# Kernel tuning notes

Measured on AMD Instinct MI355X. Metric: run time of the kernel, lower is better.

The kernel has to match this reference:

```python
import jax, jax.numpy as jnp
import numpy as np

PAD, UNK, START, END = 0, 1, 2, 3


def _lstm_scan(x_tbd, Wih, Whh, b, reverse=False):
    # x_tbd: [T,B,Din]; returns all hidden states [T,B,H] and final hidden [B,H]
    B = x_tbd.shape[1]
    Hh = Whh.shape[1]
    def step(carry, xt):
        h, c = carry
        g = xt @ Wih.T + h @ Whh.T + b  # torch gate order i,f,g,o
        i, f, gg, o = jnp.split(g, 4, axis=-1)
        c = jax.nn.sigmoid(f) * c + jax.nn.sigmoid(i) * jnp.tanh(gg)
        h = jax.nn.sigmoid(o) * jnp.tanh(c)
        return (h, c), h
    z = jnp.zeros((B, Hh), x_tbd.dtype)
    (hT, _), hs = jax.lax.scan(step, (z, z), x_tbd, reverse=reverse)
    return hs, hT


def _forward(fl, input_ids, target_ids, target_lengths):
    (emb,
     eWih0f, eWhh0f, eb0f, eWih0b, eWhh0b, eb0b,
     eWih1f, eWhh1f, eb1f, eWih1b, eWhh1b, eb1b,
     dWih0, dWhh0, db0, dWih1, dWhh1, db1,
     Wenc, Wdec, Wvoc, sW, sb, ob) = fl
    V = emb.shape[0]
    B, S = input_ids.shape
    T = target_ids.shape[1]
    D = 2 * eWhh0f.shape[1]  # decoder hidden = 2*hidden_dim
    safe = lambda ids: jnp.where(ids >= V, UNK, ids)

    # ---- bidirectional 2-layer encoder ----
    x = emb[safe(input_ids)].transpose(1, 0, 2)  # [S,B,E]
    h0f, hf0T = _lstm_scan(x, eWih0f, eWhh0f, eb0f)
    h0b, hb0T = _lstm_scan(x, eWih0b, eWhh0b, eb0b, reverse=True)
    x1 = jnp.concatenate([h0f, h0b], -1)
    h1f, hf1T = _lstm_scan(x1, eWih1f, eWhh1f, eb1f)
    h1b, hb1T = _lstm_scan(x1, eWih1b, eWhh1b, eb1b, reverse=True)
    enc_hs = jnp.concatenate([h1f, h1b], -1).transpose(1, 0, 2)  # [B,S,D]
    # decoder init hidden: concat fwd/bwd final hidden per layer -> [2,B,D]
    dec_h0 = jnp.stack([jnp.concatenate([hf0T, hb0T], -1),
                        jnp.concatenate([hf1T, hb1T], -1)])

    out_proj = jnp.tanh(emb[END:] @ Wvoc)  # [V-3, 3D]
    pad_mask = input_ids == PAD
    t_range = jnp.arange(T)

    def cell(xx, h, c, Wih, Whh, b):
        g = xx @ Wih.T + h @ Whh.T + b
        i, f, gg, o = jnp.split(g, 4, -1)
        c = jax.nn.sigmoid(f) * c + jax.nn.sigmoid(i) * jnp.tanh(gg)
        return jax.nn.sigmoid(o) * jnp.tanh(c), c

    def step(carry, xs):
        h, c, cum, hist, cur, nll = carry
        t, nt = xs  # t scalar step index, nt [B] teacher tokens
        xx = emb[cur]
        h0, c0 = cell(xx, h[0], c[0], dWih0, dWhh0, db0)
        h1, c1 = cell(h0, h[1], c[1], dWih1, dWhh1, db1)
        # intra-temporal encoder attention
        s = jnp.minimum(jnp.einsum('bd,bsd->bs', h1 @ Wenc, enc_hs), 30.0)
        e = jnp.exp(s)
        temporal = e / jnp.where(t == 0, 1.0, cum + 1e-8)
        attn = jax.nn.softmax(jnp.where(pad_mask, -jnp.inf, temporal), axis=1)
        enc_ctx = jnp.einsum('bs,bsd->bd', attn, enc_hs)
        # intra-decoder attention over previous decoder hidden states
        ds = jnp.where(t_range[None, :] < t,
                       jnp.einsum('bd,ubd->bu', h1 @ Wdec, hist), -1e9)
        dec_ctx = jnp.where(t > 0,
                            jnp.einsum('bu,ubd->bd', jax.nn.softmax(ds, axis=1), hist),
                            0.0)
        concat = jnp.concatenate([h1, enc_ctx, dec_ctx], -1)  # [B,3D]
        vocab_dist = jax.nn.softmax(concat @ out_proj.T + ob, axis=1)  # [B,V-3]
        p_gen = jax.nn.sigmoid(concat @ sW.T + sb)[:, 0]
        # generation prob of teacher token (F.pad left by END zeros)
        idx = jnp.clip(nt - END, 0, V - END - 1)
        gen_p = jnp.where((nt >= END) & (nt < V),
                          jnp.take_along_axis(vocab_dist, idx[:, None], 1)[:, 0], 0.0)
        copy_p = jnp.sum(attn * (input_ids == nt[:, None]), axis=1)
        p = p_gen * gen_p + (1.0 - p_gen) * copy_p
        nll = nll - jnp.where(t < target_lengths, jnp.log(p + 1e-9), 0.0)
        return (jnp.stack([h0, h1]), jnp.stack([c0, c1]), cum + e,
                hist.at[t].set(h1), safe(nt), nll), None

    init = (dec_h0, jnp.zeros_like(dec_h0), jnp.zeros((B, S), emb.dtype),
            jnp.zeros((T, B, D), emb.dtype),
            jnp.full((B,), START), jnp.zeros((B,), emb.dtype))
    (_, _, _, _, _, nll), _ = jax.lax.scan(step, init, (t_range, target_ids.T))
    return nll  # per-example teacher-forcing NLL, shape [B]


def setup_inputs():
    key = jax.random.key(0)
    ks = jax.random.split(key, 40)
    B, S, T = 16, 512, 128
    V, E, H = 32000, 128, 256
    D = 2 * H
    inp = {}
    inp['input_ids'] = jax.random.randint(ks[0], (B, S), 4, V)      # no pad/special ids
    inp['target_ids'] = jax.random.randint(ks[1], (B, T), 4, V)
    inp['input_lengths'] = jnp.full((B,), S, dtype=jnp.int32)       # full-length (packing is identity)
    inp['target_lengths'] = jax.random.randint(ks[2], (B,), T // 2, T + 1)
    inp['max_num_oovs'] = 0
    def xav(k, shape):
        fan = shape[0] + shape[-1]
        return jax.random.normal(k, shape, jnp.float32) * np.sqrt(2.0 / fan)
    def lstm_b(n4):
        b = np.zeros(n4, np.float32)
        b[n4 // 4:n4 // 2] = 1.0  # forget-gate bias init
        return jnp.asarray(b)
    i = 3
    inp['emb'] = jax.random.uniform(ks[i], (V, E), jnp.float32, -0.1, 0.1); i += 1
    for l, din in [(0, E), (1, D)]:
        for d in 'fb':
            inp[f'enc_Wih_l{l}{d}'] = xav(ks[i], (4 * H, din)); i += 1
            inp[f'enc_Whh_l{l}{d}'] = xav(ks[i], (4 * H, H)); i += 1
            inp[f'enc_b_l{l}{d}'] = lstm_b(4 * H)
    for l, din in [(0, E), (1, D)]:
        inp[f'dec_Wih_l{l}'] = xav(ks[i], (4 * D, din)); i += 1
        inp[f'dec_Whh_l{l}'] = xav(ks[i], (4 * D, D)); i += 1
        inp[f'dec_b_l{l}'] = lstm_b(4 * D)
    inp['Wenc_attn'] = xav(ks[i], (D, D)); i += 1
    inp['Wdec_attn'] = xav(ks[i], (D, D)); i += 1
    inp['vocab_proj'] = xav(ks[i], (E, 6 * H)); i += 1
    inp['switch_W'] = xav(ks[i], (1, 6 * H)); i += 1
    inp['switch_b'] = jnp.zeros((1,), jnp.float32)
    inp['out_bias'] = jnp.zeros((V - 3,), jnp.float32)
    return inp


def reference(input_ids, target_ids, input_lengths, target_lengths, max_num_oovs,
              emb,
              enc_Wih_l0f, enc_Whh_l0f, enc_b_l0f, enc_Wih_l0b, enc_Whh_l0b, enc_b_l0b,
              enc_Wih_l1f, enc_Whh_l1f, enc_b_l1f, enc_Wih_l1b, enc_Whh_l1b, enc_b_l1b,
              dec_Wih_l0, dec_Whh_l0, dec_b_l0, dec_Wih_l1, dec_Whh_l1, dec_b_l1,
              Wenc_attn, Wdec_attn, vocab_proj, switch_W, switch_b, out_bias):
    # input_lengths unused (all full length -> pack/pad identity); max_num_oovs only
    # widens the zero-padded tail of the generator distribution (gathered probs unchanged).
    fl = (emb,
          enc_Wih_l0f, enc_Whh_l0f, enc_b_l0f, enc_Wih_l0b, enc_Whh_l0b, enc_b_l0b,
          enc_Wih_l1f, enc_Whh_l1f, enc_b_l1f, enc_Wih_l1b, enc_Whh_l1b, enc_b_l1b,
          dec_Wih_l0, dec_Whh_l0, dec_b_l0, dec_Wih_l1, dec_Whh_l1, dec_b_l1,
          Wenc_attn, Wdec_attn, vocab_proj, switch_W, switch_b, out_bias)
    return _forward(fl, input_ids, target_ids, target_lengths)
```

## Files before the change

### kernel.cpp

```cpp
#include <hip/hip_runtime.h>
#include <hip/hip_bf16.h>
#include <math.h>

#define PAD_ID 0
#define UNK_ID 1
#define START_ID 2
#define END_ID 3

constexpr int B = 16, S = 512, T = 128, V = 32000, E = 128, H = 256, D = 512;
constexpr int C3 = 1536;
constexpr int VO = 31997;
constexpr int JS = 32000;

typedef short short8 __attribute__((ext_vector_type(8)));
typedef float f32x4 __attribute__((ext_vector_type(4)));

__device__ __forceinline__ float sigm(float x) { return 1.0f / (1.0f + __expf(-x)); }
__device__ __forceinline__ short bf16s(float x) {
    __hip_bfloat16 h = __float2bfloat16(x);
    return *reinterpret_cast<short*>(&h);
}

__device__ __forceinline__ uint4 cloadu4(const uint* p) {
    uint4 v;
    asm volatile("global_load_dwordx4 %0, %1, off sc0 sc1" : "=v"(v) : "v"(p));
    return v;
}
__device__ __forceinline__ void pstore(uint* p, uint v) {
    __hip_atomic_store(p, v, __ATOMIC_RELAXED, __HIP_MEMORY_SCOPE_AGENT);
}

__device__ __forceinline__ void gload_lds16(const void* g, void* l) {
    __builtin_amdgcn_global_load_lds(
        (const __attribute__((address_space(1))) void*)(g),
        (__attribute__((address_space(3))) void*)(l), 16, 0, 0);
}

__device__ __forceinline__ void st_bf8(ushort* dst, float4 a, float4 b) {
    short8 o;
    o[0] = bf16s(a.x); o[1] = bf16s(a.y); o[2] = bf16s(a.z); o[3] = bf16s(a.w);
    o[4] = bf16s(b.x); o[5] = bf16s(b.y); o[6] = bf16s(b.z); o[7] = bf16s(b.w);
    *(short8*)dst = o;
}

__device__ __forceinline__ void poll_stage16(const uint* src, uint e, ushort* dst) {
    uint4 a0, a1, a2, a3;
    for (;;) {
        a0 = cloadu4(src); a1 = cloadu4(src + 4); a2 = cloadu4(src + 8); a3 = cloadu4(src + 12);
        asm volatile("s_waitcnt vmcnt(0)" ::: "memory");
        __builtin_amdgcn_sched_barrier(0);
        uint d = (a0.x ^ e) | (a0.y ^ e) | (a0.z ^ e) | (a0.w ^ e)
               | (a1.x ^ e) | (a1.y ^ e) | (a1.z ^ e) | (a1.w ^ e)
               | (a2.x ^ e) | (a2.y ^ e) | (a2.z ^ e) | (a2.w ^ e)
               | (a3.x ^ e) | (a3.y ^ e) | (a3.z ^ e) | (a3.w ^ e);
        if ((d & 0xffffu) == 0) break;
        __builtin_amdgcn_s_sleep(1);
    }
    short8 o0, o1;
    o0[0] = (short)(a0.x >> 16); o0[1] = (short)(a0.y >> 16); o0[2] = (short)(a0.z >> 16); o0[3] = (short)(a0.w >> 16);
    o0[4] = (short)(a1.x >> 16); o0[5] = (short)(a1.y >> 16); o0[6] = (short)(a1.z >> 16); o0[7] = (short)(a1.w >> 16);
    o1[0] = (short)(a2.x >> 16); o1[1] = (short)(a2.y >> 16); o1[2] = (short)(a2.z >> 16); o1[3] = (short)(a2.w >> 16);
    o1[4] = (short)(a3.x >> 16); o1[5] = (short)(a3.y >> 16); o1[6] = (short)(a3.z >> 16); o1[7] = (short)(a3.w >> 16);
    *(short8*)dst = o0;
    *(short8*)(dst + 8) = o1;
}

__device__ __forceinline__ void poll_stage32(const uint* src, uint e, ushort* dst) {
    uint4 a[8];
    for (;;) {
#pragma unroll
        for (int i = 0; i < 8; i++) a[i] = cloadu4(src + i * 4);
        asm volatile("s_waitcnt vmcnt(0)" ::: "memory");
        __builtin_amdgcn_sched_barrier(0);
        uint d = 0;
#pragma unroll
        for (int i = 0; i < 8; i++)
            d |= (a[i].x ^ e) | (a[i].y ^ e) | (a[i].z ^ e) | (a[i].w ^ e);
        if ((d & 0xffffu) == 0) break;
        __builtin_amdgcn_s_sleep(1);
    }
#pragma unroll
    for (int i = 0; i < 8; i += 2) {
        short8 o;
        o[0] = (short)(a[i].x >> 16);     o[1] = (short)(a[i].y >> 16);
        o[2] = (short)(a[i].z >> 16);     o[3] = (short)(a[i].w >> 16);
        o[4] = (short)(a[i + 1].x >> 16); o[5] = (short)(a[i + 1].y >> 16);
        o[6] = (short)(a[i + 1].z >> 16); o[7] = (short)(a[i + 1].w >> 16);
        *(short8*)(dst + i * 4) = o;
    }
}

__global__ void pack4_kernel(const float* __restrict__ W, float4* __restrict__ P, int Hn, int K) {
    int i = blockIdx.x * blockDim.x + threadIdx.x;
    if (i >= K * Hn) return;
    int k = i / Hn, u = i - k * Hn;
    float4 v;
    v.x = W[(size_t)(0 * Hn + u) * K + k];
    v.y = W[(size_t)(1 * Hn + u) * K + k];
    v.z = W[(size_t)(2 * Hn + u) * K + k];
    v.w = W[(size_t)(3 * Hn + u) * K + k];
    P[(size_t)k * Hn + u] = v;
}

__global__ void packencMK_k(const float* __restrict__ W, ushort* __restrict__ P, int K) {
    int i = blockIdx.x * blockDim.x + threadIdx.x;
    if (i >= 4 * H * K) return;
    int k = i % K, row = i / K;
    int g = (row >> 3) & 3, ul = row & 7, uh = row >> 5;
    int u = uh * 8 + ul;
    P[i] = (ushort)bf16s(W[(size_t)(g * H + u) * K + k]);
}

__global__ void packdecM_k(const float* __restrict__ W, ushort* __restrict__ P) {
    int i = blockIdx.x * blockDim.x + threadIdx.x;
    if (i >= 4 * D * D) return;
    int k = i & 511, row = i >> 9;
    int g = (row >> 4) & 3, u = (row >> 6) * 16 + (row & 15);
    P[i] = (ushort)bf16s(W[(size_t)(g * D + u) * D + k]);
}

__global__ void packdecM2_k(const float* __restrict__ Wi, const float* __restrict__ Wh,
                            ushort* __restrict__ P) {
    int i = blockIdx.x * blockDim.x + threadIdx.x;
    if (i >= 4 * D * D * 2) return;
    int k = i & 1023, row = i >> 10;
    int g = (row >> 4) & 3, u = (row >> 6) * 16 + (row & 15);
    float v = (k < 512) ? Wi[(size_t)(g * D + u) * D + k]
                        : Wh[(size_t)(g * D + u) * D + (k - 512)];
    P[i] = (ushort)bf16s(v);
}

__global__ void enc0_gates2(const int* __restrict__ ids, const float* __restrict__ emb,
                            const float4* __restrict__ Pf, const float* __restrict__ bf_,
                            const float4* __restrict__ Pb, const float* __restrict__ bb_,
                            float* __restrict__ Gf, float* __restrict__ Gb) {
    int n0 = blockIdx.x * 8;
    int u = threadIdx.x;
    __shared__ float xr[8][E];
    for (int i = u; i < 8 * E; i += 256) {
        int r = i >> 7, e = i & 127;
        int n = n0 + r, s = n / B, b = n - s * B;
        int tok = ids[b * S + s];
        if (tok >= V) tok = UNK_ID;
        xr[r][e] = emb[(size_t)tok * E + e];
    }
    __syncthreads();
#pragma unroll
    for (int dir = 0; dir < 2; dir++) {
        const float4* P = dir ? Pb : Pf;
        const float* bs = dir ? bb_ : bf_;
        float* G = dir ? Gb : Gf;
        float acc[8][4];
#pragma unroll
        for (int r = 0; r < 8; r++)
#pragma unroll
            for (int g = 0; g < 4; g++) acc[r][g] = 0.f;
#pragma unroll 4
        for (int k = 0; k < E; k++) {
            float4 w = P[k * H + u];
#pragma unroll
            for (int r = 0; r < 8; r++) {
                float x = xr[r][k];
                acc[r][0] += x * w.x; acc[r][1] += x * w.y;
                acc[r][2] += x * w.z; acc[r][3] += x * w.w;
            }
        }
        float b0 = bs[u], b1 = bs[H + u], b2 = bs[2 * H + u], b3 = bs[3 * H + u];
#pragma unroll
        for (int r = 0; r < 8; r++) {
            float* g = G + (size_t)(n0 + r) * (4 * H);
            g[u] = acc[r][0] + b0; g[H + u] = acc[r][1] + b1;
// ... 136 lines not shown
                acc0 = __builtin_amdgcn_mfma_f32_16x16x32_bf16(afr[0][kt], bfr, acc0, 0, 0, 0);
                acc1 = __builtin_amdgcn_mfma_f32_16x16x32_bf16(afr[1][kt], bfr, acc1, 0, 0, 0);
            }
#pragma unroll
            for (int i = 0; i < 4; i++) {
                gs[w][hi * 4 + i][cl] = acc0[i];
                gs[w][16 + hi * 4 + i][cl] = acc1[i];
            }
        }
        __syncthreads();
        {
            float q0 = gs[gsw][0 + ul][bb];
            float q1 = gs[gsw][8 + ul][bb];
            float q2 = gs[gsw][16 + ul][bb];
            float q3 = gs[gsw][24 + ul][bb];
            float ig = sigm(pa0 + q0), fg = sigm(pa1 + q1), gt = tanhf(pa2 + q2), og = sigm(pa3 + q3);
            c_a = fg * c_a + ig * gt;
            float hA = og * tanhf(c_a);
            q0 = gs[gsw][0 + ul][bb + 8];
            q1 = gs[gsw][8 + ul][bb + 8];
            q2 = gs[gsw][16 + ul][bb + 8];
            q3 = gs[gsw][24 + ul][bb + 8];
            ig = sigm(pb0 + q0); fg = sigm(pb1 + q1); gt = tanhf(pb2 + q2); og = sigm(pb3 + q3);
            c_b = fg * c_b + ig * gt;
            float hB = og * tanhf(c_b);
            uint tg = (uint)(step + 1) & 0xffffu;
            uint* dstp = pk + (cur ^ 1) * 8192 + dirb * 4096;
            pstore(&dstp[bb * 256 + u_glob], ((uint)(ushort)bf16s(hA) << 16) | tg);
            pstore(&dstp[(bb + 8) * 256 + u_glob], ((uint)(ushort)bf16s(hB) << 16) | tg);
            ho[((size_t)(s * B + bb)) * H + u_glob] = hA;
            ho[((size_t)(s * B + bb + 8)) * H + u_glob] = hB;
            if (step == S - 1) {
                hfin[bb * (2 * H) + dirb * H + u_glob] = hA;
                hfin[(bb + 8) * (2 * H) + dirb * H + u_glob] = hB;
            }
        }
    }
}

__device__ __forceinline__ void dec0_body(int bid, char* smem,
        const int* __restrict__ tgt, const float* __restrict__ emb,
        const float4* __restrict__ P, const float* __restrict__ bias,
        float* __restrict__ G) {
    float (*xr)[E] = (float(*)[E])smem;
    int n0 = bid * 8;
    int tid = threadIdx.x;
    for (int i = tid; i < 8 * E; i += 256) {
        int r = i >> 7, e = i & 127;
        int n = n0 + r, t = n / B, b = n - t * B;
        int tok;
        if (t == 0) tok = START_ID;
        else { tok = tgt[b * T + (t - 1)]; if (tok >= V) tok = UNK_ID; }
        xr[r][e] = emb[(size_t)tok * E + e];
    }
    __syncthreads();
#pragma unroll
    for (int half = 0; half < 2; half++) {
        int u = tid + half * 256;
        float acc[8][4];
#pragma unroll
        for (int r = 0; r < 8; r++)
#pragma unroll
            for (int g = 0; g < 4; g++) acc[r][g] = 0.f;
#pragma unroll 4
        for (int k = 0; k < E; k++) {
            float4 w = P[k * D + u];
#pragma unroll
            for (int r = 0; r < 8; r++) {
                float x = xr[r][k];
                acc[r][0] += x * w.x; acc[r][1] += x * w.y;
                acc[r][2] += x * w.z; acc[r][3] += x * w.w;
            }
        }
        float b0 = bias[u], b1 = bias[D + u], b2 = bias[2 * D + u], b3 = bias[3 * D + u];
#pragma unroll
        for (int r = 0; r < 8; r++) {
            float* g = G + (size_t)(n0 + r) * (4 * D);
            g[u] = acc[r][0] + b0; g[D + u] = acc[r][1] + b1;
            g[2 * D + u] = acc[r][2] + b2; g[3 * D + u] = acc[r][3] + b3;
        }
    }
}

__device__ __forceinline__ void dec_body(int bk, char* smem,
        const float* __restrict__ G0, const ushort* __restrict__ PM0,
        const ushort* __restrict__ PM1, const float* __restrict__ b1,
        uint* __restrict__ h0pk, uint* __restrict__ h1pk,
        float* __restrict__ h1out) {
    ushort* hb = (ushort*)smem;
    float (*gs)[16][17] = (float(*)[16][17])(smem + 33024);
    int tid = threadIdx.x;
    int lane = tid & 63, w = tid >> 6;
    int cl = lane & 15, hi = lane >> 4;

    short8 a0[16], a1[32];
    {
        const ushort* base0 = PM0 + (size_t)(bk * 64 + w * 16 + cl) * 512 + hi * 8;
#pragma unroll
        for (int kt = 0; kt < 16; kt++) a0[kt] = *(const short8*)(base0 + kt * 32);
        const ushort* base1 = PM1 + (size_t)(bk * 64 + w * 16 + cl) * 1024 + hi * 8;
#pragma unroll
        for (int kt = 0; kt < 32; kt++) a1[kt] = *(const short8*)(base1 + kt * 32);
    }
    int u_loc = tid & 15, b = tid >> 4;
    int u = bk * 16 + u_loc;
    float bi0 = b1[u], bi1 = b1[512 + u], bi2 = b1[1024 + u], bi3 = b1[1536 + u];
    float c0v = 0.f, c1v = 0.f;
    int sb = tid >> 4, kseg = tid & 15;
    int sflat = sb * 512 + kseg * 32;

    for (int t = 0; t < T; t++) {
        int cur = t & 1;
        poll_stage32(h0pk + ((t + 1) & 1) * 8192 + sflat, (uint)(t + 1) & 0xffffu,
                     hb + sb * 1032 + kseg * 32);
        __syncthreads();
        {
            f32x4 acc = {0.f, 0.f, 0.f, 0.f};
            const ushort* hp = hb + cl * 1032 + hi * 8;
#pragma unroll
            for (int kt = 0; kt < 16; kt++) {
                short8 bfr = *(const short8*)(hp + kt * 32);
                acc = __builtin_amdgcn_mfma_f32_16x16x32_bf16(a0[kt], bfr, acc, 0, 0, 0);
            }
#pragma unroll
            for (int i = 0; i < 4; i++) gs[w][hi * 4 + i][cl] = acc[i];
        }
        __syncthreads();
        {
            const float* gg = G0 + ((size_t)(t * B + b)) * 2048 + u;
            float g0 = gg[0]    + gs[0][u_loc][b];
            float g1 = gg[512]  + gs[1][u_loc][b];
            float g2 = gg[1024] + gs[2][u_loc][b];
            float g3 = gg[1536] + gs[3][u_loc][b];
            float ig = sigm(g0), fg = sigm(g1), gt = tanhf(g2), og = sigm(g3);
            c0v = fg * c0v + ig * gt;
            float h0n = og * tanhf(c0v);
            pstore(&h0pk[cur * 8192 + b * 512 + u],
                   ((uint)(ushort)bf16s(h0n) << 16) | ((uint)(t + 2) & 0xffffu));
        }
        poll_stage32(h0pk + cur * 8192 + sflat, (uint)(t + 2) & 0xffffu,
                     hb + sb * 1032 + kseg * 32);
        poll_stage32(h1pk + ((t + 1) & 1) * 8192 + sflat, (uint)(t + 1) & 0xffffu,
                     hb + sb * 1032 + 512 + kseg * 32);
        __syncthreads();
        {
            f32x4 acc = {0.f, 0.f, 0.f, 0.f};
            const ushort* hp = hb + cl * 1032 + hi * 8;
#pragma unroll
            for (int kt = 0; kt < 32; kt++) {
                short8 bfr = *(const short8*)(hp + kt * 32);
                acc = __builtin_amdgcn_mfma_f32_16x16x32_bf16(a1[kt], bfr, acc, 0, 0, 0);
            }
#pragma unroll
            for (int i = 0; i < 4; i++) gs[w][hi * 4 + i][cl] = acc[i];
        }
        __syncthreads();
        {
            float g0 = bi0 + gs[0][u_loc][b];
            float g1 = bi1 + gs[1][u_loc][b];
            float g2 = bi2 + gs[2][u_loc][b];
            float g3 = bi3 + gs[3][u_loc][b];
            float ig = sigm(g0), fg = sigm(g1), gt = tanhf(g2), og = sigm(g3);
            c1v = fg * c1v + ig * gt;
            float h1n = og * tanhf(c1v);
            pstore(&h1pk[cur * 8192 + b * 512 + u],
                   ((uint)(ushort)bf16s(h1n) << 16) | ((uint)(t + 2) & 0xffffu));
            h1out[((size_t)(t * B + b)) * 512 + u] = h1n;
        }
        __syncthreads();
    }
}

__device__ __forceinline__ void encht2_body(int bid,
        const float* __restrict__ h1f, const float* __restrict__ h1b,
        ushort* __restrict__ enchB) {
    int idx = bid * 256 + threadIdx.x;
    int b = idx >> 15;
    int r = idx & 32767;
    int o = r >> 9, s = r & 511;
    const float* src = (o < 32) ? (h1f + ((size_t)(s * B + b)) * H + o * 8)
                                : (h1b + ((size_t)(s * B + b)) * H + (o - 32) * 8);
    float4 v0 = *(const float4*)src, v1 = *(const float4*)(src + 4);
    st_bf8(enchB + ((size_t)b << 18) + o * 4096 + s * 8, v0, v1);
}

__device__ __forceinline__ void encht2T_body(int bid,
        const float* __restrict__ h1f, const float* __restrict__ h1b,
        ushort* __restrict__ enchT) {
    int idx = bid * 256 + threadIdx.x;
    int b = idx >> 15;
    int r = idx & 32767;
    int o = r >> 9, d = r & 511;
    float f[8];
#pragma unroll
    for (int j = 0; j < 8; j++) {
        int s = o * 8 + j;
        f[j] = (d < H) ? h1f[((size_t)(s * B + b)) * H + d]
                       : h1b[((size_t)(s * B + b)) * H + (d - H)];
    }
    float4 v0 = {f[0], f[1], f[2], f[3]}, v1 = {f[4], f[5], f[6], f[7]};
    st_bf8(enchT + ((size_t)b << 18) + o * 4096 + d * 8, v0, v1);
}

__device__ __forceinline__ void outproj_body(int bid, char* smem,
        const float* __restrict__ emb, const float* __restrict__ Wvoc,
        __hip_bfloat16* __restrict__ outT2) {
    float (*er)[E + 1] = (float(*)[E + 1])smem;
    int j0 = bid * 32;
    int jl = threadIdx.x & 31, oq = threadIdx.x >> 5;
    for (int i = threadIdx.x; i < 32 * E; i += 256) {
        int jj = i >> 7, e = i & 127;
        int j = j0 + jj;
        er[jj][e] = (j < VO) ? emb[(size_t)(3 + j) * E + e] : 0.f;
    }
    __syncthreads();
    int j = j0 + jl;
#pragma unroll 1
    for (int i = 0; i < 24; i++) {
        int o = oq * 24 + i;
        int k0 = o * 8;
        float acc[8];
#pragma unroll
        for (int kk = 0; kk < 8; kk++) acc[kk] = 0.f;
#pragma unroll 4
        for (int e = 0; e < E; e++) {
            float x = er[jl][e];
            float4 w0 = *(const float4*)(Wvoc + (size_t)e * C3 + k0);
            float4 w1 = *(const float4*)(Wvoc + (size_t)e * C3 + k0 + 4);
            acc[0] += x * w0.x; acc[1] += x * w0.y; acc[2] += x * w0.z; acc[3] += x * w0.w;
            acc[4] += x * w1.x; acc[5] += x * w1.y; acc[6] += x * w1.z; acc[7] += x * w1.w;
        }
        short8 v;
#pragma unroll
        for (int kk = 0; kk < 8; kk++) v[kk] = bf16s(tanhf(acc[kk]));
        *reinterpret_cast<short8*>((char*)outT2 + ((size_t)o * JS + j) * 16) = v;
    }
}

template<int NF, int TILES, int OSTR, bool DOEXP>
__device__ __forceinline__ void gemm16_body(char* smem,
        const ushort* __restrict__ Abase, int arow_stride,
        const ushort* __restrict__ Bsrc, float* __restrict__ outbase,
        int out_stride) {
    ushort* Bs = (ushort*)smem;
    const int CH = NF * 64;
    const int NG = CH / 64;
    int tid = threadIdx.x;
    int lane = tid & 63, w = tid >> 6;
    int cl = lane & 15, hi = lane >> 4;
    short8 a[NF];
    {
        const ushort* asrc = Abase + (size_t)(w * 16 + cl) * arow_stride + hi * 8;
#pragma unroll
        for (int kt = 0; kt < NF; kt++) a[kt] = *(const short8*)(asrc + kt * 32);
    }
    for (int g = w; g < NG; g += 8) {
        int c = g * 64 + lane;
        int o = c >> 4, jl = c & 15;
        gload_lds16(Bsrc + ((size_t)o * OSTR + jl) * 8,
                    (char*)Bs + (size_t)(g * 64) * 16);
    }
    asm volatile("s_waitcnt vmcnt(0)" ::: "memory");
    __syncthreads();
    int buf = 0;
    for (int t = 0; t < TILES; t++) {
        if (t + 1 < TILES) {
            for (int g = w; g < NG; g += 8) {
                int c = g * 64 + lane;
                int o = c >> 4, jl = c & 15;
                gload_lds16(Bsrc + ((size_t)o * OSTR + (t + 1) * 16 + jl) * 8,
                            (char*)Bs + (size_t)((buf ^ 1) * CH + g * 64) * 16);
            }
        }
        f32x4 acc = {0.f, 0.f, 0.f, 0.f};
        const ushort* bp = Bs + (size_t)buf * CH * 8 + (size_t)(hi * 16 + cl) * 8;
#pragma unroll
        for (int kt = 0; kt < NF; kt++) {
            short8 b = *(const short8*)(bp + (size_t)kt * 512);
            acc = __builtin_amdgcn_mfma_f32_16x16x32_bf16(a[kt], b, acc, 0, 0, 0);
        }
#pragma unroll
        for (int i = 0; i < 4; i++) {
            int row = w * 16 + hi * 4 + i;
            float v = acc[i];
            if (DOEXP) v = __expf(fminf(v, 30.0f));
            outbase[(size_t)row * out_stride + t * 16 + cl] = v;
        }
        asm volatile("s_waitcnt vmcnt(0)" ::: "memory");
        __syncthreads();
        buf ^= 1;
    }
}


__global__ void __launch_bounds__(256) megaA(
        const float* Gf, const float* Gb, const ushort* PMf, const ushort* PMb,
        float* hof, float* hob, float* hfin, uint* pk,
        const int* tgt, const float* emb, const float4* PdW, const float* dbias,
        float* Gd0) {
    __shared__ __align__(16) char smem[17152];
    int blk = blockIdx.x;
    if (blk < 16) enc_scan_body(blk, smem, Gf, Gb, PMf, PMb, hof, hob, hfin, pk);
    else dec0_body(blk - 16, smem, tgt, emb, PdW, dbias, Gd0);
}

__global__ void __launch_bounds__(256) enc_pscan3(
        const float* Gf, const float* Gb, const ushort* PMf, const ushort* PMb,
        float* hof, float* hob, float* hfin, uint* pk) {
    __shared__ __align__(16) char smem[17152];
    enc_scan_body(blockIdx.x, smem, Gf, Gb, PMf, PMb, hof, hob, hfin, pk);
}

__global__ void __launch_bounds__(256) megaC(
        const float* G0, const ushort* PM0, const ushort* PM1, const float* b1,
        uint* h0pk, uint* h1pk, float* h1out,
        const float* h1f, const float* h1b, ushort* enchB, ushort* enchT,
        const float* emb, const float* Wvoc, __hip_bfloat16* outT2) {
    __shared__ __align__(16) char smem[37376];
    int blk = blockIdx.x;
    if (blk < 32) dec_body(blk, smem, G0, PM0, PM1, b1, h0pk, h1pk, h1out);
    else if (blk < 2080) encht2_body(blk - 32, h1f, h1b, enchB);
    else if (blk < 4128) encht2T_body(blk - 2080, h1f, h1b, enchT);
    else outproj_body(blk - 4128, smem, emb, Wvoc, outT2);
}

__global__ void dec_initpk(const float* __restrict__ hinit,
                           uint* __restrict__ h0pk, uint* __restrict__ h1pk) {
    int i = blockIdx.x * blockDim.x + threadIdx.x;
    if (i >= B * D) return;
    pstore(&h0pk[8192 + i], ((uint)(ushort)bf16s(hinit[i]) << 16) | 1u);
    pstore(&h1pk[8192 + i], ((uint)(ushort)bf16s(hinit[B * D + i]) << 16) | 1u);
}

__global__ void qproj(const float* __restrict__ h1d, const float* __restrict__ Wenc,
                      const float* __restrict__ Wdec, ushort* __restrict__ qeb16,
                      ushort* __restrict__ qdb16, ushort* __restrict__ h1dB1) {
    int n = blockIdx.x;
    int o = threadIdx.x;
    __shared__ float hr[D];
    hr[o] = h1d[(size_t)n * D + o];
    __syncthreads();
    float ae = 0.f, ad = 0.f;
#pragma unroll 4
    for (int k = 0; k < D; k++) {
        float hk = hr[k];
        ae += hk * Wenc[k * D + o];
        ad += hk * Wdec[k * D + o];
    }
    int b = n & 15, t = n >> 4;
    size_t rowb = (size_t)(b * 128 + t) << 9;
    qeb16[rowb + o] = (ushort)bf16s(ae);
    qdb16[rowb + o] = (ushort)bf16s(ad);
    if (o < 64) {
        float4 v0 = *(const float4*)(hr + o * 8);
        float4 v1 = *(const float4*)(hr + o * 8 + 4);
        st_bf8(h1dB1 + ((size_t)b << 16) + o * 1024 + t * 8, v0, v1);
    }
}

__global__ void pack_h1dB2(const float* __restrict__ h1d, ushort* __restrict__ h1dB2) {
    int idx = blockIdx.x * 256 + threadIdx.x;
    int b = idx >> 13;
    int r = idx & 8191;
    int o = r >> 9, d = r & 511;
    float f[8];
#pragma unroll
    for (int j = 0; j < 8; j++)
        f[j] = h1d[((size_t)((o * 8 + j) * B + b)) * D + d];
    float4 v0 = {f[0], f[1], f[2], f[3]}, v1 = {f[4], f[5], f[6], f[7]};
    st_bf8(h1dB2 + ((size_t)b << 16) + o * 4096 + d * 8, v0, v1);
}

__global__ void __launch_bounds__(512) scoreAB(
        const ushort* __restrict__ qeb16, const ushort* __restrict__ enchB,
        float* __restrict__ ew,
        const ushort* __restrict__ qdb16, const ushort* __restrict__ h1dB1,
        float* __restrict__ dsout) {
    __shared__ __align__(16) char smem[32768];
    int blk = blockIdx.x;
    if (blk < 16) {
        int b = blk;
        gemm16_body<16, 32, 512, true>(smem,
            qeb16 + ((size_t)(b * 128) << 9), 512,
            enchB + ((size_t)b << 18),
            ew + (size_t)b * T * S, S);
    } else {
        int b = blk - 16;
        gemm16_body<16, 8, 128, false>(smem,
            qdb16 + ((size_t)(b * 128) << 9), 512,
            h1dB1 + ((size_t)b << 16),
            dsout + ((size_t)(b * 128)) * 128, 128);
    }
}

__global__ void temporal_k(float* __restrict__ ew) {
    int i = blockIdx.x * blockDim.x + threadIdx.x;
    if (i >= B * S) return;
    int b = i / S, sx = i - b * S;
    float cum = 0.f;
    for (int t = 0; t < T; t++) {
        size_t idx = ((size_t)(b * T + t)) * S + sx;
        float v = ew[idx];
        ew[idx] = v / (t == 0 ? 1.0f : (cum + 1e-8f));
        cum += v;
    }
}

__global__ void __launch_bounds__(512) smAB(
        const float* __restrict__ ew, const int* __restrict__ ids,
        const int* __restrict__ tgt, ushort* __restrict__ awb16,
        float* __restrict__ copyp,
        const float* __restrict__ dsout, ushort* __restrict__ pdb16) {
    __shared__ float red[512];
    int blk = blockIdx.x;
// ... 192 lines not shown
        float mn = fmaxf(M, mq);
        SS = SS * __expf(M - mn) + sq * __expf(mq - mn);
        M = mn;
        GL = fmaxf(GL, gq);
    }
    int nt = tgt[row];
    float genp = (nt >= 3 && nt < V) ? __expf(GL - M) / SS : 0.f;
    float pg = pgen[row];
    float p = pg * genp + (1.f - pg) * copyp[row];
    __shared__ float red[128];
    red[t] = (t < tlen[b]) ? -logf(p + 1e-9f) : 0.f;
    __syncthreads();
    for (int w = 64; w > 0; w >>= 1) { if (t < w) red[t] += red[t + w]; __syncthreads(); }
    if (t == 0) out[b] = red[0];
}

extern "C" void kernel_launch(void* const* d_in, const int* in_sizes, int n_in,
                              void* d_out, int out_size, void* d_ws, size_t ws_size,
                              hipStream_t stream) {
    const int* input_ids = (const int*)d_in[0];
    const int* target_ids = (const int*)d_in[1];
    const int* tlen = (const int*)d_in[3];
    const float* emb = (const float*)d_in[5];
    const float* eWih0f = (const float*)d_in[6],  *eWhh0f = (const float*)d_in[7],  *eb0f = (const float*)d_in[8];
    const float* eWih0b = (const float*)d_in[9],  *eWhh0b = (const float*)d_in[10], *eb0b = (const float*)d_in[11];
    const float* eWih1f = (const float*)d_in[12], *eWhh1f = (const float*)d_in[13], *eb1f = (const float*)d_in[14];
    const float* eWih1b = (const float*)d_in[15], *eWhh1b = (const float*)d_in[16], *eb1b = (const float*)d_in[17];
    const float* dWih0 = (const float*)d_in[18], *dWhh0 = (const float*)d_in[19], *db0 = (const float*)d_in[20];
    const float* dWih1 = (const float*)d_in[21], *dWhh1 = (const float*)d_in[22], *db1 = (const float*)d_in[23];
    const float* Wenc = (const float*)d_in[24], *Wdec = (const float*)d_in[25];
    const float* Wvoc = (const float*)d_in[26], *sW = (const float*)d_in[27], *sb = (const float*)d_in[28];
    const float* ob = (const float*)d_in[29];
    float* out = (float*)d_out;
    (void)ws_size; (void)n_in; (void)in_sizes; (void)out_size;

    char* A = (char*)d_ws;
    float4* pWih0f = (float4*)(A + 0);
    float4* pWih0b = (float4*)(A + 524288);
    ushort* PMW1f  = (ushort*)(A + 1048576);
    ushort* PMW1b  = (ushort*)(A + 2097152);
    float4* pdWih0 = (float4*)(A + 5242880);
    ushort* PMf0  = (ushort*)(A + 6291456);
    ushort* PMb0  = (ushort*)(A + 6815744);
    ushort* PMf1  = (ushort*)(A + 7340032);
    ushort* PMb1  = (ushort*)(A + 7864320);
    float* G0f = (float*)(A + 23068672);
    float* G0b = (float*)(A + 56623104);
    __hip_bfloat16* outT2 = (__hip_bfloat16*)A;

    char* Bh = A + 98304000;
    float* h0f = (float*)(Bh + 0);
    float* h0b = (float*)(Bh + 8388608);
    float* h1d = (float*)(Bh + 0);
    ushort* qeb16 = (ushort*)(Bh + 4194304);
    ushort* awb16 = (ushort*)(Bh + 6291456);
    ushort* qdb16 = (ushort*)(Bh + 8388608);
    ushort* h1dB1 = (ushort*)(Bh + 10485760);
    float* ew  = (float*)(Bh + 12582912);
    float* pbuf = (float*)(Bh + 12582912);

    char* Cr = Bh + 16777216;
    float* h1f = (float*)(Cr + 0);
    float* h1b = (float*)(Cr + 8388608);
    ushort* ccb16 = (ushort*)(Cr + 16777216);
    float*  dsout = (float*)(Cr + 23068672);
    ushort* pdb16 = (ushort*)(Cr + 24117248);
    ushort* h1dB2 = (ushort*)(Cr + 24641536);
    float* dec_init = (float*)(Cr + 29360128);
    float* pgen  = (float*)(Cr + 29425664);
    float* copyp = (float*)(Cr + 29433856);
    uint* hpkE0  = (uint*)(Cr + 29769728);
    uint* hpkE1  = (uint*)(Cr + 29835264);
    uint* h0pkD  = (uint*)(Cr + 29900800);
    uint* h1pkD  = (uint*)(Cr + 29966336);

    char* X = Cr + 30031872;
    float*  Gd0x  = (float*)(X + 0);
    ushort* PM0x  = (ushort*)(X + 16777216);
    ushort* PM1x  = (ushort*)(X + 18874368);
    ushort* enchB = (ushort*)(X + 23068672);
    float*  ectx  = (float*)(X + 31457280);
    float*  dctx  = (float*)(X + 35651584);
    ushort* enchT = (ushort*)(X + 39845888);

    hipMemsetAsync(hpkE0, 0, 262144, stream);

    auto pack = [&](const float* W, float4* P, int Hn, int K) {
        int total = Hn * K;
        hipLaunchKernelGGL(pack4_kernel, dim3((total + 255) / 256), dim3(256), 0, stream, W, P, Hn, K);
    };
    pack(eWih0f, pWih0f, H, E);
    pack(eWih0b, pWih0b, H, E);
    pack(dWih0, pdWih0, D, E);
    hipLaunchKernelGGL(packencMK_k, dim3(4 * H * 256 / 256), dim3(256), 0, stream, eWhh0f, PMf0, 256);
    hipLaunchKernelGGL(packencMK_k, dim3(4 * H * 256 / 256), dim3(256), 0, stream, eWhh0b, PMb0, 256);
    hipLaunchKernelGGL(packencMK_k, dim3(4 * H * 256 / 256), dim3(256), 0, stream, eWhh1f, PMf1, 256);
    hipLaunchKernelGGL(packencMK_k, dim3(4 * H * 256 / 256), dim3(256), 0, stream, eWhh1b, PMb1, 256);
    hipLaunchKernelGGL(packencMK_k, dim3(4 * H * 512 / 256), dim3(256), 0, stream, eWih1f, PMW1f, 512);
    hipLaunchKernelGGL(packencMK_k, dim3(4 * H * 512 / 256), dim3(256), 0, stream, eWih1b, PMW1b, 512);
    hipLaunchKernelGGL(packdecM_k, dim3(4 * D * D / 256), dim3(256), 0, stream, dWhh0, PM0x);
    hipLaunchKernelGGL(packdecM2_k, dim3(8 * D * D / 256), dim3(256), 0, stream, dWih1, dWhh1, PM1x);

    hipLaunchKernelGGL(enc0_gates2, dim3(S * B / 8), dim3(256), 0, stream,
                       input_ids, emb, pWih0f, eb0f, pWih0b, eb0b, G0f, G0b);
    hipLaunchKernelGGL(megaA, dim3(272), dim3(256), 0, stream,
                       G0f, G0b, PMf0, PMb0, h0f, h0b, dec_init, hpkE0,
                       target_ids, emb, pdWih0, db0, Gd0x);
    hipLaunchKernelGGL(enc1g_mfma, dim3(256), dim3(256), 0, stream,
                       h0f, h0b, PMW1f, PMW1b, eb1f, eb1b, G0f, G0b);
    hipLaunchKernelGGL(enc_pscan3, dim3(16), dim3(256), 0, stream,
                       G0f, G0b, PMf1, PMb1, h1f, h1b, dec_init + B * D, hpkE1);
    hipLaunchKernelGGL(dec_initpk, dim3(B * D / 256), dim3(256), 0, stream,
                       dec_init, h0pkD, h1pkD);
    hipLaunchKernelGGL(megaC, dim3(5128), dim3(256), 0, stream,
                       Gd0x, PM0x, PM1x, db1, h0pkD, h1pkD, h1d,
                       h1f, h1b, enchB, enchT, emb, Wvoc, outT2);
    hipLaunchKernelGGL(qproj, dim3(T * B), dim3(D), 0, stream,
                       h1d, Wenc, Wdec, qeb16, qdb16, h1dB1);
    hipLaunchKernelGGL(pack_h1dB2, dim3(512), dim3(256), 0, stream, h1d, h1dB2);
    hipLaunchKernelGGL(scoreAB, dim3(32), dim3(512), 0, stream,
                       qeb16, enchB, ew, qdb16, h1dB1, dsout);
    hipLaunchKernelGGL(temporal_k, dim3((B * S + 255) / 256), dim3(256), 0, stream, ew);
    hipLaunchKernelGGL(smAB, dim3(4096), dim3(512), 0, stream,
                       ew, input_ids, target_ids, awb16, copyp, dsout, pdb16);
    hipLaunchKernelGGL(ctxAB, dim3(32), dim3(512), 0, stream,
                       awb16, enchT, ectx, pdb16, h1dB2, dctx);
    hipLaunchKernelGGL(concat_k, dim3(B * T), dim3(D), 0, stream,
                       h1d, ectx, dctx, sW, sb, ccb16, pgen);
    hipLaunchKernelGGL(vocab_mfma3, dim3(256), dim3(512), 0, stream,
                       outT2, ccb16, ob, target_ids, pbuf);
    hipLaunchKernelGGL(combine_nll_k, dim3(B), dim3(T), 0, stream,
                       pbuf, target_ids, pgen, copyp, tlen, out);
}
```

Baseline: 4.003 ms.

## Skew decoder LSTM layers so layer-0 step t+1 overlaps layer-1 step t

Restructures the two-layer decoder recurrence into a wavefront schedule. Layer 0's first step is precomputed in a new dec_init2 kernel. Each loop iteration then polls both layers' packed hidden states in one pass and runs the layer-1 step t together with the layer-0 step t+1 in a single fused MFMA loop. This cuts per-step grid-wide polling and barrier rounds from three to one and shares the B-fragment LDS reads between the two matmuls, at the cost of extra shared memory and a small serial fp32 init kernel.

Result: no change. 4.002 ms (-0.0%).

```diff
diff --git a/kernel.cpp b/kernel.cpp
--- a/kernel.cpp
+++ b/kernel.cpp
@@ -65,16 +65,19 @@
     *(short8*)(dst + 8) = o1;
 }
 
-__device__ __forceinline__ void poll_stage32(const uint* src, uint e, ushort* dst) {
-    uint4 a[8];
+__device__ __forceinline__ void poll_stage32x2(const uint* s0, const uint* s1, uint e,
+                                               ushort* d0, ushort* d1) {
+    uint4 a[16];
     for (;;) {
 #pragma unroll
-        for (int i = 0; i < 8; i++) a[i] = cloadu4(src + i * 4);
+        for (int i = 0; i < 8; i++) a[i] = cloadu4(s0 + i * 4);
+#pragma unroll
+        for (int i = 0; i < 8; i++) a[8 + i] = cloadu4(s1 + i * 4);
         asm volatile("s_waitcnt vmcnt(0)" ::: "memory");
         __builtin_amdgcn_sched_barrier(0);
         uint d = 0;
 #pragma unroll
-        for (int i = 0; i < 8; i++)
+        for (int i = 0; i < 16; i++)
             d |= (a[i].x ^ e) | (a[i].y ^ e) | (a[i].z ^ e) | (a[i].w ^ e);
         if ((d & 0xffffu) == 0) break;
         __builtin_amdgcn_s_sleep(1);
@@ -86,7 +89,16 @@
         o[2] = (short)(a[i].z >> 16);     o[3] = (short)(a[i].w >> 16);
         o[4] = (short)(a[i + 1].x >> 16); o[5] = (short)(a[i + 1].y >> 16);
         o[6] = (short)(a[i + 1].z >> 16); o[7] = (short)(a[i + 1].w >> 16);
-        *(short8*)(dst + i * 4) = o;
+        *(short8*)(d0 + i * 4) = o;
+    }
+#pragma unroll
+    for (int i = 0; i < 8; i += 2) {
+        short8 o;
+        o[0] = (short)(a[8 + i].x >> 16);     o[1] = (short)(a[8 + i].y >> 16);
+        o[2] = (short)(a[8 + i].z >> 16);     o[3] = (short)(a[8 + i].w >> 16);
+        o[4] = (short)(a[8 + i + 1].x >> 16); o[5] = (short)(a[8 + i + 1].y >> 16);
+        o[6] = (short)(a[8 + i + 1].z >> 16); o[7] = (short)(a[8 + i + 1].w >> 16);
+        *(short8*)(d1 + i * 4) = o;
     }
 }
 
@@ -393,9 +405,10 @@
         const float* __restrict__ G0, const ushort* __restrict__ PM0,
         const ushort* __restrict__ PM1, const float* __restrict__ b1,
         uint* __restrict__ h0pk, uint* __restrict__ h1pk,
-        float* __restrict__ h1out) {
+        const float* __restrict__ c0a, float* __restrict__ h1out) {
     ushort* hb = (ushort*)smem;
-    float (*gs)[16][17] = (float(*)[16][17])(smem + 33024);
+    float (*gs0)[16][17] = (float(*)[16][17])(smem + 33024);
+    float (*gs1)[16][17] = (float(*)[16][17])(smem + 37376);
     int tid = threadIdx.x;
     int lane = tid & 63, w = tid >> 6;
     int cl = lane & 15, hi = lane >> 4;
@@ -412,67 +425,63 @@
     int u_loc = tid & 15, b = tid >> 4;
     int u = bk * 16 + u_loc;
     float bi0 = b1[u], bi1 = b1[512 + u], bi2 = b1[1024 + u], bi3 = b1[1536 + u];
-    float c0v = 0.f, c1v = 0.f;
+    float c0v = c0a[b * 512 + u];
+    float c1v = 0.f;
     int sb = tid >> 4, kseg = tid & 15;
     int sflat = sb * 512 + kseg * 32;
 
-    for (int t = 0; t < T; t++) {
-        int cur = t & 1;
-        poll_stage32(h0pk + ((t + 1) & 1) * 8192 + sflat, (uint)(t + 1) & 0xffffu,
-                     hb + sb * 1032 + kseg * 32);
+    for (int r = 0; r < T; r++) {
+        int tn = (r + 1 < T) ? (r + 1) : (T - 1);
+        const float* gg = G0 + ((size_t)(tn * B + b)) * 2048 + u;
+        float p0 = gg[0], p1 = gg[512], p2 = gg[1024], p3 = gg[1536];
+        poll_stage32x2(h0pk + ((r + 1) & 1) * 8192 + sflat,
+                       h1pk + ((r + 1) & 1) * 8192 + sflat,
+                       (uint)(r + 1) & 0xffffu,
+                       hb + sb * 1032 + kseg * 32,
+                       hb + sb * 1032 + 512 + kseg * 32);
         __syncthreads();
         {
-            f32x4 acc = {0.f, 0.f, 0.f, 0.f};
-            const ushort* hp = hb + cl * 1032 + hi * 8;
-#pragma unroll
-            for (int kt = 0; kt < 16; kt++) {
-                short8 bfr = *(const short8*)(hp + kt * 32);
-                acc = __builtin_amdgcn_mfma_f32_16x16x32_bf16(a0[kt], bfr, acc, 0, 0, 0);
-            }
-#pragma unroll
-            for (int i = 0; i < 4; i++) gs[w][hi * 4 + i][cl] = acc[i];
-        }
-        __syncthreads();
-        {
-            const float* gg = G0 + ((size_t)(t * B + b)) * 2048 + u;
-            float g0 = gg[0]    + gs[0][u_loc][b];
-            float g1 = gg[512]  + gs[1][u_loc][b];
-            float g2 = gg[1024] + gs[2][u_loc][b];
-            float g3 = gg[1536] + gs[3][u_loc][b];
-            float ig = sigm(g0), fg = sigm(g1), gt = tanhf(g2), og = sigm(g3);
-            c0v = fg * c0v + ig * gt;
-            float h0n = og * tanhf(c0v);
-            pstore(&h0pk[cur * 8192 + b * 512 + u],
-                   ((uint)(ushort)bf16s(h0n) << 16) | ((uint)(t + 2) & 0xffffu));
-        }
-        poll_stage32(h0pk + cur * 8192 + sflat, (uint)(t + 2) & 0xffffu,
-                     hb + sb * 1032 + kseg * 32);
-        poll_stage32(h1pk + ((t + 1) & 1) * 8192 + sflat, (uint)(t + 1) & 0xffffu,
-                     hb + sb * 1032 + 512 + kseg * 32);
-        __syncthreads();
-        {
-            f32x4 acc = {0.f, 0.f, 0.f, 0.f};
+            f32x4 acc1 = {0.f, 0.f, 0.f, 0.f};
+            f32x4 acc0 = {0.f, 0.f, 0.f, 0.f};
             const ushort* hp = hb + cl * 1032 + hi * 8;
 #pragma unroll
             for (int kt = 0; kt < 32; kt++) {
                 short8 bfr = *(const short8*)(hp + kt * 32);
-                acc = __builtin_amdgcn_mfma_f32_16x16x32_bf16(a1[kt], bfr, acc, 0, 0, 0);
-            }
-#pragma unroll
-            for (int i = 0; i < 4; i++) gs[w][hi * 4 + i][cl] = acc[i];
+                acc1 = __builtin_amdgcn_mfma_f32_16x16x32_bf16(a1[kt], bfr, acc1, 0, 0, 0);
+                if (kt < 16)
+                    acc0 = __builtin_amdgcn_mfma_f32_16x16x32_bf16(a0[kt], bfr, acc0, 0, 0, 0);
+            }
+#pragma unroll
+            for (int i = 0; i < 4; i++) {
+                gs1[w][hi * 4 + i][cl] = acc1[i];
+                gs0[w][hi * 4 + i][cl] = acc0[i];
+            }
         }
         __syncthreads();
         {
-            float g0 = bi0 + gs[0][u_loc][b];
-            float g1 = bi1 + gs[1][u_loc][b];
-            float g2 = bi2 + gs[2][u_loc][b];
-            float g3 = bi3 + gs[3][u_loc][b];
+            uint tg = (uint)(r + 2) & 0xffffu;
+            int pp = r & 1;
+            float g0 = bi0 + gs1[0][u_loc][b];
+            float g1 = bi1 + gs1[1][u_loc][b];
+            float g2 = bi2 + gs1[2][u_loc][b];
+            float g3 = bi3 + gs1[3][u_loc][b];
             float ig = sigm(g0), fg = sigm(g1), gt = tanhf(g2), og = sigm(g3);
             c1v = fg * c1v + ig * gt;
             float h1n = og * tanhf(c1v);
-            pstore(&h1pk[cur * 8192 + b * 512 + u],
-                   ((uint)(ushort)bf16s(h1n) << 16) | ((uint)(t + 2) & 0xffffu));
-            h1out[((size_t)(t * B + b)) * 512 + u] = h1n;
+            pstore(&h1pk[pp * 8192 + b * 512 + u],
+                   ((uint)(ushort)bf16s(h1n) << 16) | tg);
+            h1out[((size_t)(r * B + b)) * 512 + u] = h1n;
+            if (r + 1 < T) {
+                g0 = p0 + gs0[0][u_loc][b];
+                g1 = p1 + gs0[1][u_loc][b];
+                g2 = p2 + gs0[2][u_loc][b];
+                g3 = p3 + gs0[3][u_loc][b];
+                ig = sigm(g0); fg = sigm(g1); gt = tanhf(g2); og = sigm(g3);
+                c0v = fg * c0v + ig * gt;
+                float h0n = og * tanhf(c0v);
+                pstore(&h0pk[pp * 8192 + b * 512 + u],
+                       ((uint)(ushort)bf16s(h0n) << 16) | tg);
+            }
         }
         __syncthreads();
     }
@@ -618,25 +627,57 @@
     enc_scan_body(blockIdx.x, smem, Gf, Gb, PMf, PMb, hof, hob, hfin, pk);
 }
 
+__global__ void __launch_bounds__(256) dec_init2(
+        const float* __restrict__ Gd0, const float* __restrict__ dWhh0,
+        const float* __restrict__ hinit, uint* __restrict__ h0pk,
+        float* __restrict__ c0a) {
+    __shared__ float hr[D];
+    int b = blockIdx.x;
+    int tid = threadIdx.x;
+    hr[tid] = hinit[b * 512 + tid];
+    hr[tid + 256] = hinit[b * 512 + tid + 256];
+    __syncthreads();
+#pragma unroll
+    for (int half = 0; half < 2; half++) {
+        int u = tid + half * 256;
+        float acc[4] = {0.f, 0.f, 0.f, 0.f};
+#pragma unroll
+        for (int g = 0; g < 4; g++) {
+            const float* wr = dWhh0 + (size_t)(g * 512 + u) * 512;
+            float s = 0.f;
+#pragma unroll 4
+            for (int k = 0; k < 512; k++) s += wr[k] * hr[k];
+            acc[g] = s;
+        }
+        const float* gg = Gd0 + ((size_t)(0 * B + b)) * 2048 + u;
+        float g0 = gg[0] + acc[0], g1 = gg[512] + acc[1];
+        float g2 = gg[1024] + acc[2], g3 = gg[1536] + acc[3];
+        float ig = sigm(g0), fg = sigm(g1), gt = tanhf(g2), og = sigm(g3);
+        (void)fg;
+        float c0 = ig * gt;
+        float h00 = og * tanhf(c0);
+        c0a[b * 512 + u] = c0;
+        pstore(&h0pk[8192 + b * 512 + u], ((uint)(ushort)bf16s(h00) << 16) | 1u);
+    }
+}
+
 __global__ void __launch_bounds__(256) megaC(
         const float* G0, const ushort* PM0, const ushort* PM1, const float* b1,
-        uint* h0pk, uint* h1pk, float* h1out,
+        uint* h0pk, uint* h1pk, const float* c0a, float* h1out,
+        const float* hinit,
         const float* h1f, const float* h1b, ushort* enchB, ushort* enchT,
         const float* emb, const float* Wvoc, __hip_bfloat16* outT2) {
-    __shared__ __align__(16) char smem[37376];
+    __shared__ __align__(16) char smem[41728];
     int blk = blockIdx.x;
-    if (blk < 32) dec_body(blk, smem, G0, PM0, PM1, b1, h0pk, h1pk, h1out);
-    else if (blk < 2080) encht2_body(blk - 32, h1f, h1b, enchB);
-    else if (blk < 4128) encht2T_body(blk - 2080, h1f, h1b, enchT);
-    else outproj_body(blk - 4128, smem, emb, Wvoc, outT2);
-}
-
-__global__ void dec_initpk(const float* __restrict__ hinit,
-                           uint* __restrict__ h0pk, uint* __restrict__ h1pk) {
-    int i = blockIdx.x * blockDim.x + threadIdx.x;
-    if (i >= B * D) return;
-    pstore(&h0pk[8192 + i], ((uint)(ushort)bf16s(hinit[i]) << 16) | 1u);
-    pstore(&h1pk[8192 + i], ((uint)(ushort)bf16s(hinit[B * D + i]) << 16) | 1u);
+    if (blk < 32) dec_body(blk, smem, G0, PM0, PM1, b1, h0pk, h1pk, c0a, h1out);
+    else if (blk < 64) {
+        int idx = (blk - 32) * 256 + threadIdx.x;
+        pstore(&h1pk[8192 + idx],
+               ((uint)(ushort)bf16s(hinit[B * D + idx]) << 16) | 1u);
+    }
+    else if (blk < 2112) encht2_body(blk - 64, h1f, h1b, enchB);
+    else if (blk < 4160) encht2T_body(blk - 2112, h1f, h1b, enchT);
+    else outproj_body(blk - 4160, smem, emb, Wvoc, outT2);
 }
 
 __global__ void qproj(const float* __restrict__ h1d, const float* __restrict__ Wenc,
@@ -995,6 +1036,7 @@
     float*  ectx  = (float*)(X + 31457280);
     float*  dctx  = (float*)(X + 35651584);
     ushort* enchT = (ushort*)(X + 39845888);
+    float*  c0a   = (float*)(X + 48234496);
 
     hipMemsetAsync(hpkE0, 0, 262144, stream);
 
@@ -1019,15 +1061,15 @@
     hipLaunchKernelGGL(megaA, dim3(272), dim3(256), 0, stream,
                        G0f, G0b, PMf0, PMb0, h0f, h0b, dec_init, hpkE0,
                        target_ids, emb, pdWih0, db0, Gd0x);
+    hipLaunchKernelGGL(dec_init2, dim3(16), dim3(256), 0, stream,
+                       Gd0x, dWhh0, dec_init, h0pkD, c0a);
     hipLaunchKernelGGL(enc1g_mfma, dim3(256), dim3(256), 0, stream,
                        h0f, h0b, PMW1f, PMW1b, eb1f, eb1b, G0f, G0b);
     hipLaunchKernelGGL(enc_pscan3, dim3(16), dim3(256), 0, stream,
                        G0f, G0b, PMf1, PMb1, h1f, h1b, dec_init + B * D, hpkE1);
-    hipLaunchKernelGGL(dec_initpk, dim3(B * D / 256), dim3(256), 0, stream,
-                       dec_init, h0pkD, h1pkD);
-    hipLaunchKernelGGL(megaC, dim3(5128), dim3(256), 0, stream,
-                       Gd0x, PM0x, PM1x, db1, h0pkD, h1pkD, h1d,
-                       h1f, h1b, enchB, enchT, emb, Wvoc, outT2);
+    hipLaunchKernelGGL(megaC, dim3(5160), dim3(256), 0, stream,
+                       Gd0x, PM0x, PM1x, db1, h0pkD, h1pkD, c0a, h1d,
+                       dec_init, h1f, h1b, enchB, enchT, emb, Wvoc, outT2);
     hipLaunchKernelGGL(qproj, dim3(T * B), dim3(D), 0, stream,
                        h1d, Wenc, Wdec, qeb16, qdb16, h1dB1);
     hipLaunchKernelGGL(pack_h1dB2, dim3(512), dim3(256), 0, stream, h1d, h1dB2);
```

## Split decoder layers into separate kernels, overlapping layer-0 recurrence with encoder layer-1 scan

Applied to the files above, without the earlier changes.

The fused two-layer decoder recurrence is split. The layer-0 scan now runs in the same launch as the encoder layer-1 scan, which is possible because layer 0 only needs the precomputed decoder gate inputs and the encoder layer-0 final state. Layer-0 hidden states are written to a bf16 history buffer that the layer-1 scan reads in the later mega-kernel, and the separate init-pack kernel is folded into both launches. This takes the layer-0 latency off the serial critical path. The cost is extra global traffic for the h0 history and cross-block polling alongside the encoder scan.

After: 3.775 ms. 5.7% less time.

```diff
diff --git a/kernel.cpp b/kernel.cpp
--- a/kernel.cpp
+++ b/kernel.cpp
@@ -389,41 +389,33 @@
     }
 }
 
-__device__ __forceinline__ void dec_body(int bk, char* smem,
+__device__ __forceinline__ void decL0_body(int bk, char* smem,
         const float* __restrict__ G0, const ushort* __restrict__ PM0,
-        const ushort* __restrict__ PM1, const float* __restrict__ b1,
-        uint* __restrict__ h0pk, uint* __restrict__ h1pk,
-        float* __restrict__ h1out) {
+        uint* __restrict__ h0pk, ushort* __restrict__ h0bf) {
     ushort* hb = (ushort*)smem;
-    float (*gs)[16][17] = (float(*)[16][17])(smem + 33024);
+    float (*gs)[16][17] = (float(*)[16][17])(smem + 16640);
     int tid = threadIdx.x;
     int lane = tid & 63, w = tid >> 6;
     int cl = lane & 15, hi = lane >> 4;
-
-    short8 a0[16], a1[32];
+    short8 a0[16];
     {
         const ushort* base0 = PM0 + (size_t)(bk * 64 + w * 16 + cl) * 512 + hi * 8;
 #pragma unroll
         for (int kt = 0; kt < 16; kt++) a0[kt] = *(const short8*)(base0 + kt * 32);
-        const ushort* base1 = PM1 + (size_t)(bk * 64 + w * 16 + cl) * 1024 + hi * 8;
-#pragma unroll
-        for (int kt = 0; kt < 32; kt++) a1[kt] = *(const short8*)(base1 + kt * 32);
     }
     int u_loc = tid & 15, b = tid >> 4;
     int u = bk * 16 + u_loc;
-    float bi0 = b1[u], bi1 = b1[512 + u], bi2 = b1[1024 + u], bi3 = b1[1536 + u];
-    float c0v = 0.f, c1v = 0.f;
+    float c0v = 0.f;
     int sb = tid >> 4, kseg = tid & 15;
     int sflat = sb * 512 + kseg * 32;
 
     for (int t = 0; t < T; t++) {
-        int cur = t & 1;
         poll_stage32(h0pk + ((t + 1) & 1) * 8192 + sflat, (uint)(t + 1) & 0xffffu,
-                     hb + sb * 1032 + kseg * 32);
+                     hb + sb * 520 + kseg * 32);
         __syncthreads();
         {
             f32x4 acc = {0.f, 0.f, 0.f, 0.f};
-            const ushort* hp = hb + cl * 1032 + hi * 8;
+            const ushort* hp = hb + cl * 520 + hi * 8;
 #pragma unroll
             for (int kt = 0; kt < 16; kt++) {
                 short8 bfr = *(const short8*)(hp + kt * 32);
@@ -442,11 +434,44 @@
             float ig = sigm(g0), fg = sigm(g1), gt = tanhf(g2), og = sigm(g3);
             c0v = fg * c0v + ig * gt;
             float h0n = og * tanhf(c0v);
-            pstore(&h0pk[cur * 8192 + b * 512 + u],
-                   ((uint)(ushort)bf16s(h0n) << 16) | ((uint)(t + 2) & 0xffffu));
-        }
-        poll_stage32(h0pk + cur * 8192 + sflat, (uint)(t + 2) & 0xffffu,
-                     hb + sb * 1032 + kseg * 32);
+            ushort hb16 = (ushort)bf16s(h0n);
+            pstore(&h0pk[(t & 1) * 8192 + b * 512 + u],
+                   ((uint)hb16 << 16) | ((uint)(t + 2) & 0xffffu));
+            h0bf[(size_t)t * 8192 + b * 512 + u] = hb16;
+        }
+        __syncthreads();
+    }
+}
+
+__device__ __forceinline__ void decL1_body(int bk, char* smem,
+        const ushort* __restrict__ PM1, const float* __restrict__ b1,
+        const ushort* __restrict__ h0bf, uint* __restrict__ h1pk,
+        float* __restrict__ h1out) {
+    ushort* hb = (ushort*)smem;
+    float (*gs)[16][17] = (float(*)[16][17])(smem + 33024);
+    int tid = threadIdx.x;
+    int lane = tid & 63, w = tid >> 6;
+    int cl = lane & 15, hi = lane >> 4;
+    short8 a1[32];
+    {
+        const ushort* base1 = PM1 + (size_t)(bk * 64 + w * 16 + cl) * 1024 + hi * 8;
+#pragma unroll
+        for (int kt = 0; kt < 32; kt++) a1[kt] = *(const short8*)(base1 + kt * 32);
+    }
+    int u_loc = tid & 15, b = tid >> 4;
+    int u = bk * 16 + u_loc;
+    float bi0 = b1[u], bi1 = b1[512 + u], bi2 = b1[1024 + u], bi3 = b1[1536 + u];
+    float c1v = 0.f;
+    int sb = tid >> 4, kseg = tid & 15;
+    int sflat = sb * 512 + kseg * 32;
+
+    for (int t = 0; t < T; t++) {
+        {
+            const short8* src = (const short8*)(h0bf + (size_t)t * 8192 + sflat);
+            short8 v0 = src[0], v1 = src[1], v2 = src[2], v3 = src[3];
+            short8* dst = (short8*)(hb + sb * 1032 + kseg * 32);
+            dst[0] = v0; dst[1] = v1; dst[2] = v2; dst[3] = v3;
+        }
         poll_stage32(h1pk + ((t + 1) & 1) * 8192 + sflat, (uint)(t + 1) & 0xffffu,
                      hb + sb * 1032 + 512 + kseg * 32);
         __syncthreads();
@@ -470,7 +495,7 @@
             float ig = sigm(g0), fg = sigm(g1), gt = tanhf(g2), og = sigm(g3);
             c1v = fg * c1v + ig * gt;
             float h1n = og * tanhf(c1v);
-            pstore(&h1pk[cur * 8192 + b * 512 + u],
+            pstore(&h1pk[(t & 1) * 8192 + b * 512 + u],
                    ((uint)(ushort)bf16s(h1n) << 16) | ((uint)(t + 2) & 0xffffu));
             h1out[((size_t)(t * B + b)) * 512 + u] = h1n;
         }
@@ -611,32 +636,38 @@
     else dec0_body(blk - 16, smem, tgt, emb, PdW, dbias, Gd0);
 }
 
-__global__ void __launch_bounds__(256) enc_pscan3(
+__global__ void __launch_bounds__(256) megaB2(
         const float* Gf, const float* Gb, const ushort* PMf, const ushort* PMb,
-        float* hof, float* hob, float* hfin, uint* pk) {
-    __shared__ __align__(16) char smem[17152];
-    enc_scan_body(blockIdx.x, smem, Gf, Gb, PMf, PMb, hof, hob, hfin, pk);
-}
-
-__global__ void __launch_bounds__(256) megaC(
-        const float* G0, const ushort* PM0, const ushort* PM1, const float* b1,
-        uint* h0pk, uint* h1pk, float* h1out,
+        float* hof, float* hob, float* hfin, uint* pkE,
+        const float* Gd0, const ushort* PM0, uint* h0pk, ushort* h0bf,
+        const float* hinit) {
+    __shared__ __align__(16) char smem[20992];
+    int blk = blockIdx.x;
+    if (blk < 16) enc_scan_body(blk, smem, Gf, Gb, PMf, PMb, hof, hob, hfin, pkE);
+    else if (blk < 48) decL0_body(blk - 16, smem, Gd0, PM0, h0pk, h0bf);
+    else {
+        int idx = (blk - 48) * 256 + threadIdx.x;
+        pstore(&h0pk[8192 + idx],
+               ((uint)(ushort)bf16s(hinit[idx]) << 16) | 1u);
+    }
+}
+
+__global__ void __launch_bounds__(256) megaC2(
+        const ushort* PM1, const float* b1, const ushort* h0bf,
+        uint* h1pk, float* h1out, const float* hinit,
         const float* h1f, const float* h1b, ushort* enchB, ushort* enchT,
         const float* emb, const float* Wvoc, __hip_bfloat16* outT2) {
     __shared__ __align__(16) char smem[37376];
     int blk = blockIdx.x;
-    if (blk < 32) dec_body(blk, smem, G0, PM0, PM1, b1, h0pk, h1pk, h1out);
-    else if (blk < 2080) encht2_body(blk - 32, h1f, h1b, enchB);
-    else if (blk < 4128) encht2T_body(blk - 2080, h1f, h1b, enchT);
-    else outproj_body(blk - 4128, smem, emb, Wvoc, outT2);
-}
-
-__global__ void dec_initpk(const float* __restrict__ hinit,
-                           uint* __restrict__ h0pk, uint* __restrict__ h1pk) {
-    int i = blockIdx.x * blockDim.x + threadIdx.x;
-    if (i >= B * D) return;
-    pstore(&h0pk[8192 + i], ((uint)(ushort)bf16s(hinit[i]) << 16) | 1u);
-    pstore(&h1pk[8192 + i], ((uint)(ushort)bf16s(hinit[B * D + i]) << 16) | 1u);
+    if (blk < 32) decL1_body(blk, smem, PM1, b1, h0bf, h1pk, h1out);
+    else if (blk < 64) {
+        int idx = (blk - 32) * 256 + threadIdx.x;
+        pstore(&h1pk[8192 + idx],
+               ((uint)(ushort)bf16s(hinit[B * D + idx]) << 16) | 1u);
+    }
+    else if (blk < 2112) encht2_body(blk - 64, h1f, h1b, enchB);
+    else if (blk < 4160) encht2T_body(blk - 2112, h1f, h1b, enchT);
+    else outproj_body(blk - 4160, smem, emb, Wvoc, outT2);
 }
 
 __global__ void qproj(const float* __restrict__ h1d, const float* __restrict__ Wenc,
@@ -995,6 +1026,7 @@
     float*  ectx  = (float*)(X + 31457280);
     float*  dctx  = (float*)(X + 35651584);
     ushort* enchT = (ushort*)(X + 39845888);
+    ushort* h0bf  = (ushort*)(X + 48234496);
 
     hipMemsetAsync(hpkE0, 0, 262144, stream);
 
@@ -1021,12 +1053,11 @@
                        target_ids, emb, pdWih0, db0, Gd0x);
     hipLaunchKernelGGL(enc1g_mfma, dim3(256), dim3(256), 0, stream,
                        h0f, h0b, PMW1f, PMW1b, eb1f, eb1b, G0f, G0b);
-    hipLaunchKernelGGL(enc_pscan3, dim3(16), dim3(256), 0, stream,
-                       G0f, G0b, PMf1, PMb1, h1f, h1b, dec_init + B * D, hpkE1);
-    hipLaunchKernelGGL(dec_initpk, dim3(B * D / 256), dim3(256), 0, stream,
-                       dec_init, h0pkD, h1pkD);
-    hipLaunchKernelGGL(megaC, dim3(5128), dim3(256), 0, stream,
-                       Gd0x, PM0x, PM1x, db1, h0pkD, h1pkD, h1d,
+    hipLaunchKernelGGL(megaB2, dim3(80), dim3(256), 0, stream,
+                       G0f, G0b, PMf1, PMb1, h1f, h1b, dec_init + B * D, hpkE1,
+                       Gd0x, PM0x, h0pkD, h0bf, dec_init);
+    hipLaunchKernelGGL(megaC2, dim3(5160), dim3(256), 0, stream,
+                       PM1x, db1, h0bf, h1pkD, h1d, dec_init,
                        h1f, h1b, enchB, enchT, emb, Wvoc, outT2);
     hipLaunchKernelGGL(qproj, dim3(T * B), dim3(D), 0, stream,
                        h1d, Wenc, Wdec, qeb16, qdb16, h1dB1);
```
